# Optimization experiments

Measured on AMD Instinct MI355X. Metric: run time of the kernel, lower is better.

The kernel has to match this reference:

```python
import jax, jax.numpy as jnp
import numpy as np

B, S, E, R = 64, 2048, 256, 50


def setup_inputs() -> dict:
    key = jax.random.key(0)
    ks = jax.random.split(key, 22)
    n = lambda k, shp, s=0.05: (jax.random.normal(k, shp, jnp.float32) * s)
    d = {
        "encoder_o": jax.random.normal(ks[0], (B, S, E), jnp.float32),
        "h0": jax.random.normal(ks[1], (1, B, E), jnp.float32),
        "c0": jax.random.normal(ks[2], (1, B, E), jnp.float32),
        "r_in": jax.random.randint(ks[3], (B,), 0, R),
        "k1": jax.random.randint(ks[4], (B, 1), 0, S),
        "k2": jax.random.randint(ks[5], (B, 1), 0, S),
        "W_ih": n(ks[6], (4 * E, E)),
        "W_hh": n(ks[7], (4 * E, E)),
        "b_ih": n(ks[8], (4 * E,)),
        "b_hh": n(ks[9], (4 * E,)),
        "W_attn": n(ks[10], (E, 2 * E)),
        "b_attn": n(ks[11], (E,)),
        "W_conv": n(ks[12], (E, 2 * E, 3)),
        "b_conv": n(ks[13], (E,)),
        "sos_emb": n(ks[14], (1, E)),
        "rel_emb": n(ks[15], (R, E)),
        "W_rel": n(ks[16], (R, E)),
        "b_rel": n(ks[17], (R,)),
        "W_ent1": n(ks[18], (1, E)),
        "b_ent1": n(ks[19], (1,)),
        "W_ent2": n(ks[20], (1, E)),
        "b_ent2": n(ks[21], (1,)),
    }
    return d


def reference(encoder_o, h0, c0, r_in, k1, k2, W_ih, W_hh, b_ih, b_hh,
              W_attn, b_attn, W_conv, b_conv, sos_emb, rel_emb,
              W_rel, b_rel, W_ent1, b_ent1, W_ent2, b_ent2):
    Bx, Sx, Ex = encoder_o.shape

    def lstm_step(x, h, c):  # single decode step, x/h/c: [B,E]
        gates = x @ W_ih.T + h @ W_hh.T + (b_ih + b_hh)  # [B,4E]
        i, f, g, o = jnp.split(gates, 4, axis=-1)        # PyTorch gate order i,f,g,o
        c2 = jax.nn.sigmoid(f) * c + jax.nn.sigmoid(i) * jnp.tanh(g)
        h2 = jax.nn.sigmoid(o) * jnp.tanh(c2)
        return h2, c2

    def attend(q):  # Luong dot attention + tanh(linear(cat(mix,q))); q: [B,E]
        scores = jnp.einsum('be,bse->bs', q, encoder_o)
        attn = jax.nn.softmax(scores, axis=-1)
        mix = jnp.einsum('bs,bse->be', attn, encoder_o)
        comb = jnp.concatenate([mix, q], axis=-1)        # [B,2E]
        return jnp.tanh(comb @ W_attn.T + b_attn)

    def step(x, h, c):
        h2, c2 = lstm_step(x, h, c)
        return attend(h2), h2, c2

    kern = jnp.transpose(W_conv, (2, 1, 0))  # [3, 2E, E] for NWC/WIO

    def ent_heads(o):  # o: [B,E]
        vec = jnp.broadcast_to(o[:, None, :], (Bx, Sx, Ex))  # seq_and_vec
        feat = jnp.concatenate([encoder_o, vec], axis=-1)    # [B,S,2E]
        conv = jax.lax.conv_general_dilated(
            feat, kern, (1,), 'SAME',
            dimension_numbers=('NWC', 'WIO', 'NWC')) + b_conv
        conv = jax.nn.relu(conv)                             # [B,S,E]
        e1 = conv @ W_ent1.T + b_ent1                        # [B,S,1]
        e2 = conv @ W_ent2.T + b_ent2
        return e1, e2

    h, c = h0[0], c0[0]
    # t1: <sos> -> relation logits
    x = jnp.broadcast_to(sos_emb[0], (Bx, Ex))
    out1, h, c = step(x, h, c)
    t1_out = out1 @ W_rel.T + b_rel                          # [B,R]
    # t2: relation embedding -> entity-1 span heads
    out2, h, c = step(rel_emb[r_in], h, c)
    e1a, e2a = ent_heads(out2)
    # t3: gathered k1+k2 encoder vectors -> entity-2 span heads
    idx = jnp.arange(Bx)
    kk = encoder_o[idx, k1[:, 0]] + encoder_o[idx, k2[:, 0]]  # vectorized seq_gather
    out3, h, c = step(kk, h, c)
    e1b, e2b = ent_heads(out3)
    # pack outputs: [B, R + 4*S]
    return jnp.concatenate(
        [t1_out, e1a[..., 0], e2a[..., 0], e1b[..., 0], e2b[..., 0]], axis=1)
```

## Files before the change

kernel.cpp:

```cpp
#include <hip/hip_runtime.h>
#include <hip/hip_bf16.h>

#define EE 256
#define SS 2048
#define BB 64
#define RN 50
#define OSTR 8242

typedef __attribute__((ext_vector_type(4))) float vf4;
typedef __attribute__((ext_vector_type(8))) short s8v;
typedef __attribute__((ext_vector_type(4))) short s4v;
typedef __attribute__((ext_vector_type(4))) unsigned short u16x4;
typedef __attribute__((ext_vector_type(2))) unsigned int u32x2;

__device__ __forceinline__ unsigned short f2bf(float f){
  __hip_bfloat16 h = __float2bfloat16(f);
  return *reinterpret_cast<unsigned short*>(&h);
}
__device__ __forceinline__ unsigned int f2bf2(float a, float b){
  __hip_bfloat162 h = __float22bfloat162_rn(make_float2(a, b));
  return *reinterpret_cast<unsigned int*>(&h);
}
__device__ __forceinline__ float sigm(float x){ return 1.0f/(1.0f + __expf(-x)); }
__device__ __forceinline__ float dot4(vf4 a, vf4 b){ return a.x*b.x + a.y*b.y + a.z*b.z + a.w*b.w; }

__device__ __forceinline__ vf4 mfma16(s4v a, s4v b, vf4 c){
#if __has_builtin(__builtin_amdgcn_mfma_f32_16x16x16bf16_1k)
  return __builtin_amdgcn_mfma_f32_16x16x16bf16_1k(a, b, c, 0, 0, 0);
#else
  vf4 d;
  asm volatile("v_mfma_f32_16x16x16_bf16 %0, %1, %2, %3\n\ts_nop 7\n\ts_nop 7"
               : "=v"(d) : "v"(a), "v"(b), "v"(c));
  return d;
#endif
}

__global__ __launch_bounds__(256) void k_pre(
  const float* __restrict__ enc, const float* __restrict__ h0, const float* __restrict__ c0,
  const int* __restrict__ r_in, const int* __restrict__ k1, const int* __restrict__ k2,
  const float* __restrict__ sos, const float* __restrict__ rel,
  float* __restrict__ xT, float* __restrict__ hT0, float* __restrict__ cT)
{
  int bid = blockIdx.x, t = threadIdx.x;
  int part = bid >> 6, b = bid & 63;
  if (part == 0){
    xT[(size_t)0*EE*BB + t*BB + b] = sos[t];
  } else if (part == 1){
    xT[(size_t)1*EE*BB + t*BB + b] = rel[r_in[b]*EE + t];
  } else if (part == 2){
    int i1 = k1[b], i2 = k2[b];
    xT[(size_t)2*EE*BB + t*BB + b] =
      enc[((size_t)b*SS + i1)*EE + t] + enc[((size_t)b*SS + i2)*EE + t];
  } else {
    hT0[t*BB + b] = h0[b*EE + t];
    cT [t*BB + b] = c0[b*EE + t];
  }
}

__global__ __launch_bounds__(256) void k_step(
  const float* __restrict__ hT_cur, const float* __restrict__ xT_st,
  const float* __restrict__ W_ih, const float* __restrict__ W_hh,
  const float* __restrict__ b_ih, const float* __restrict__ b_hh,
  float* __restrict__ cT, float* __restrict__ hT_next, float* __restrict__ hs_st)
{
  int e = blockIdx.x, tid = threadIdx.x;
  int w = tid >> 6, b = tid & 63;
  int grow = w*EE + e;
  const float* wh = W_hh + (size_t)grow*EE;
  const float* wi = W_ih + (size_t)grow*EE;
  float acc = b_ih[grow] + b_hh[grow];
  #pragma unroll 4
  for (int k4 = 0; k4 < EE/4; ++k4){
    vf4 wh4 = *(const vf4*)(wh + k4*4);
    vf4 wi4 = *(const vf4*)(wi + k4*4);
    int k = k4*4;
    acc += hT_cur[(k+0)*BB+b]*wh4.x + hT_cur[(k+1)*BB+b]*wh4.y
         + hT_cur[(k+2)*BB+b]*wh4.z + hT_cur[(k+3)*BB+b]*wh4.w;
    acc += xT_st[(k+0)*BB+b]*wi4.x + xT_st[(k+1)*BB+b]*wi4.y
         + xT_st[(k+2)*BB+b]*wi4.z + xT_st[(k+3)*BB+b]*wi4.w;
  }
  __shared__ float sm[4][BB];
  sm[w][b] = acc;
  __syncthreads();
  if (tid < BB){
    float iv = sm[0][tid], fv = sm[1][tid], gv = sm[2][tid], ov = sm[3][tid];
    float cprev = cT[e*BB + tid];
    float cn = sigm(fv)*cprev + sigm(iv)*tanhf(gv);
    float hn = sigm(ov)*tanhf(cn);
    cT[e*BB + tid] = cn;
    hT_next[e*BB + tid] = hn;
    hs_st[(size_t)tid*EE + e] = hn;
  }
}

__global__ __launch_bounds__(256) void k_wprep(const float* __restrict__ W_conv,
                                               unsigned short* __restrict__ WT)
{
  int o = blockIdx.x, tid = threadIdx.x;
  for (int r = tid; r < 768; r += 256)
    WT[(size_t)r*EE + o] = f2bf(W_conv[(size_t)o*1536 + 768 + r]);
}

__global__ __launch_bounds__(256) void k_attend(
  const float* __restrict__ enc, const float* __restrict__ hs,
  float* __restrict__ mixc, float* __restrict__ stats)
{
  int bid = blockIdx.x; int b = bid >> 3, ch = bid & 7;
  int tid = threadIdx.x, lane = tid & 63, wv = tid >> 6;
  __shared__ float hsm[3][EE];
  __shared__ float wgt[3][256];
  __shared__ float red[3][4];
  __shared__ float mg[3];
  __shared__ vf4 mpart[4][3][64];
  for (int i = tid; i < 3*EE; i += 256) hsm[i>>8][i&255] = hs[((size_t)(i>>8)*BB + b)*EE + (i&255)];
  __syncthreads();
  int s = ch*256 + tid;
  const vf4* er = (const vf4*)(enc + ((size_t)b*SS + s)*EE);
  const vf4* q0 = (const vf4*)hsm[0];
  const vf4* q1 = (const vf4*)hsm[1];
  const vf4* q2 = (const vf4*)hsm[2];
  float a0=0.f, a1=0.f, a2=0.f;
  #pragma unroll 8
  for (int k = 0; k < EE/4; ++k){
    vf4 ev = er[k];
    a0 += dot4(ev, q0[k]);
    a1 += dot4(ev, q1[k]);
    a2 += dot4(ev, q2[k]);
  }
  float m0=a0, m1=a1, m2=a2;
  #pragma unroll
  for (int d=1; d<64; d<<=1){
    m0 = fmaxf(m0, __shfl_xor(m0,d));
    m1 = fmaxf(m1, __shfl_xor(m1,d));
    m2 = fmaxf(m2, __shfl_xor(m2,d));
  }
  if (lane==0){ red[0][wv]=m0; red[1][wv]=m1; red[2][wv]=m2; }
  __syncthreads();
  if (tid < 3) mg[tid] = fmaxf(fmaxf(red[tid][0],red[tid][1]), fmaxf(red[tid][2],red[tid][3]));
  __syncthreads();
  float e0 = __expf(a0-mg[0]), e1 = __expf(a1-mg[1]), e2 = __expf(a2-mg[2]);
  wgt[0][tid]=e0; wgt[1][tid]=e1; wgt[2][tid]=e2;
  #pragma unroll
  for (int d=1; d<64; d<<=1){
    e0 += __shfl_xor(e0,d); e1 += __shfl_xor(e1,d); e2 += __shfl_xor(e2,d);
  }
  if (lane==0){ red[0][wv]=e0; red[1][wv]=e1; red[2][wv]=e2; }
  __syncthreads();
  if (tid < 3){
    float l = red[tid][0]+red[tid][1]+red[tid][2]+red[tid][3];
    int o = ((tid*BB + b)*8 + ch)*2;
    stats[o] = mg[tid]; stats[o+1] = l;
  }
  __syncthreads();
  vf4 A0 = (vf4)0.0f, A1 = (vf4)0.0f, A2 = (vf4)0.0f;
  for (int i=0;i<64;++i){
    int sl = wv*64 + i;
    vf4 ev = *(const vf4*)(enc + ((size_t)b*SS + ch*256 + sl)*EE + lane*4);
    A0 += ev*wgt[0][sl]; A1 += ev*wgt[1][sl]; A2 += ev*wgt[2][sl];
  }
  mpart[wv][0][lane]=A0; mpart[wv][1][lane]=A1; mpart[wv][2][lane]=A2;
  __syncthreads();
  if (tid < 192){
    int q = tid >> 6, e4 = tid & 63;
    vf4 sum = mpart[0][q][e4] + mpart[1][q][e4] + mpart[2][q][e4] + mpart[3][q][e4];
    *(vf4*)(mixc + ((size_t)(q*BB+b)*8 + ch)*EE + e4*4) = sum;
  }
}

__global__ __launch_bounds__(256) void k_post(
  const float* __restrict__ mixc, const float* __restrict__ hs,
  const float* __restrict__ stats,
  const float* __restrict__ W_attn, const float* __restrict__ b_attn,
  const float* __restrict__ W_rel, const float* __restrict__ b_rel,
  const unsigned short* __restrict__ WT, const float* __restrict__ b_conv,
  float* __restrict__ out, float* __restrict__ vv)
{
  int b = blockIdx.x, t = threadIdx.x;
  __shared__ float comb[3][2*EE];
  __shared__ float o1[EE], o2s[EE], o3s[EE];
  #pragma unroll
  for (int q=0;q<3;q++){
    float M = -1e30f;
    #pragma unroll
    for (int c=0;c<8;c++) M = fmaxf(M, stats[((q*BB+b)*8 + c)*2]);
    float L = 0.f;
    float scl[8];
    #pragma unroll
    for (int c=0;c<8;c++){
      int o = ((q*BB+b)*8 + c)*2;
      float e = __expf(stats[o]-M);
      scl[c] = e; L += stats[o+1]*e;
    }
    float invL = 1.0f/L;
    float m = 0.f;
    #pragma unroll
    for (int c=0;c<8;c++) m += mixc[((size_t)(q*BB+b)*8 + c)*EE + t] * scl[c];
    comb[q][t] = m * invL;
    comb[q][EE+t] = hs[((size_t)q*BB + b)*EE + t];
  }
  __syncthreads();
  float a0 = b_attn[t], a1 = a0, a2 = a0;
  const vf4* wr = (const vf4*)(W_attn + (size_t)t*2*EE);
  const vf4* c0v = (const vf4*)comb[0];
  const vf4* c1v = (const vf4*)comb[1];
  const vf4* c2v = (const vf4*)comb[2];
  #pragma unroll 4
  for (int k=0;k<2*EE/4;++k){
    vf4 w = wr[k];
    a0 += dot4(w, c0v[k]); a1 += dot4(w, c1v[k]); a2 += dot4(w, c2v[k]);
  }
  o1[t]=tanhf(a0); o2s[t]=tanhf(a1); o3s[t]=tanhf(a2);
  __syncthreads();
  if (t < RN){
    float acc = b_rel[t];
    const vf4* wrel = (const vf4*)(W_rel + (size_t)t*EE);
    const vf4* ov = (const vf4*)o1;
    for (int k=0;k<EE/4;++k) acc += dot4(wrel[k], ov[k]);
    out[(size_t)b*OSTR + t] = acc;
  }
  float va0=0,va1=0,va2=0, vb0=0,vb1=0,vb2=0;
  for (int i=0;i<EE;++i){
    float x2 = o2s[i], x3 = o3s[i];
    const unsigned short* wt = WT + (size_t)i*3*EE + t;
    float w0 = __uint_as_float(((unsigned int)wt[0]) << 16);
    float w1 = __uint_as_float(((unsigned int)wt[EE]) << 16);
    float w2 = __uint_as_float(((unsigned int)wt[2*EE]) << 16);
    va0 += x2*w0; va1 += x2*w1; va2 += x2*w2;
    vb0 += x3*w0; vb1 += x3*w1; vb2 += x3*w2;
  }
  float bc = b_conv[t];
  vv[((0*3+0)*BB + b)*EE + t] = va0+va1+va2+bc;
  vv[((0*3+1)*BB + b)*EE + t] = va1+va2+bc;
  vv[((0*3+2)*BB + b)*EE + t] = va0+va1+bc;
  vv[((1*3+0)*BB + b)*EE + t] = vb0+vb1+vb2+bc;
  vv[((1*3+1)*BB + b)*EE + t] = vb1+vb2+bc;
  vv[((1*3+2)*BB + b)*EE + t] = vb0+vb1+bc;
}

__global__ __launch_bounds__(256) void k_bprep(const float* __restrict__ W_conv,
                                               unsigned short* __restrict__ Bp)
{
  int gid = blockIdx.x*256 + threadIdx.x;
  int kc  = gid >> 10;
  int rem = gid & 1023;
  int ni  = rem >> 6;
  int l   = rem & 63;
  int o   = ni*16 + (l & 15);
  int kbase = kc*32 + ((l >> 4) << 3);
  u16x4 lo4, hi4;
  #pragma unroll
  for (int j=0;j<8;++j){
    int k = kbase + j; int ktap = k >> 8; int i = k & 255;
    unsigned short v = f2bf(W_conv[((size_t)o*512 + i)*3 + ktap]);
    if (j<4){ if(j==0)lo4.x=v; else if(j==1)lo4.y=v; else if(j==2)lo4.z=v; else lo4.w=v; }
    else    { if(j==4)hi4.x=v; else if(j==5)hi4.y=v; else if(j==6)hi4.z=v; else hi4.w=v; }
  }
  u16x4* dst = (u16x4*)(Bp + (size_t)gid*8);
  dst[0] = lo4; dst[1] = hi4;
}

__global__ __launch_bounds__(256, 3) void k_conv(
  const float* __restrict__ enc, const unsigned short* __restrict__ Bp,
  const float* __restrict__ vv,
  const float* __restrict__ W_e1, const float* __restrict__ b_e1,
  const float* __restrict__ W_e2, const float* __restrict__ b_e2,
  float* __restrict__ out)
{
  int stile = blockIdx.x, b = blockIdx.y;
  int s0 = stile*64;
  int tid = threadIdx.x, lane = tid & 63, w = tid >> 6;
  int lo = lane & 15, hi = lane >> 4;
  __shared__ __align__(16) unsigned short Ab[66*256];
  __shared__ float part2[4][64][4];

  {
    const float* eb = enc + (size_t)b*SS*EE;
    for (int idx = tid; idx < 66*64; idx += 256){
      int r = idx >> 6, c4 = idx & 63;
      int s = s0 - 1 + r;
      vf4 v = (vf4)0.0f;
      if (s >= 0 && s < SS) v = *(const vf4*)(eb + (size_t)s*EE + c4*4);
      u32x2 pk; pk.x = f2bf2(v.x, v.y); pk.y = f2bf2(v.z, v.w);
      int byte = (r*512 + c4*8) ^ ((r & 7) << 4);
      *(u32x2*)((char*)Ab + byte) = pk;
    }
  }
  __syncthreads();

  vf4 acc[4][4];
  #pragma unroll
  for (int oi=0;oi<4;++oi){
    #pragma unroll
    for (int si=0;si<4;++si) acc[oi][si] = (vf4)0.0f;
  }
  const s8v* Bp8 = (const s8v*)Bp;
  s8v bf[4], bfn[4];
  #pragma unroll
  for (int oi=0;oi<4;++oi) bf[oi] = Bp8[((0*16 + (w*4+oi)) << 6) + lane];

  for (int kc=0; kc<24; ++kc){
    int ktap = kc >> 3;
    int colb = ((kc & 7) << 6) + (hi << 4);
    s8v af[4];
    #pragma unroll
    for (int si=0;si<4;++si){
      int row = si*16 + lo + ktap;
      int byte = row*512 + (colb ^ ((row & 7) << 4));
      af[si] = *(const s8v*)((const char*)Ab + byte);
    }
    if (kc < 23){
      #pragma unroll
      for (int oi=0;oi<4;++oi) bfn[oi] = Bp8[(((kc+1)*16 + (w*4+oi)) << 6) + lane];
    }
    #pragma unroll
    for (int oi=0;oi<4;++oi){
      #pragma unroll
      for (int si=0;si<4;++si)
        acc[oi][si] = __builtin_amdgcn_mfma_f32_16x16x32_bf16(bf[oi], af[si], acc[oi][si], 0, 0, 0);
    }
    #pragma unroll
    for (int oi=0;oi<4;++oi) bf[oi] = bfn[oi];
  }

  bool firstTile = (s0 == 0), lastTile = (s0 + 64 == SS);
  vf4 vaI[4], vbI[4]; s4v aw[4];
  #pragma unroll
  for (int oi=0;oi<4;++oi){
    int o4 = w*64 + oi*16 + hi*4;
    vaI[oi] = *(const vf4*)(vv + ((0*3+0)*BB + b)*EE + o4);
    vbI[oi] = *(const vf4*)(vv + ((1*3+0)*BB + b)*EE + o4);
    vf4 w1 = *(const vf4*)(W_e1 + o4);
    vf4 w2 = *(const vf4*)(W_e2 + o4);
    float e0 = (lo==0) ? w1.x : ((lo==1) ? w2.x : 0.0f);
    float e1 = (lo==0) ? w1.y : ((lo==1) ? w2.y : 0.0f);
    float e2 = (lo==0) ? w1.z : ((lo==1) ? w2.z : 0.0f);
    float e3 = (lo==0) ? w1.w : ((lo==1) ? w2.w : 0.0f);
    u32x2 t; t.x = f2bf2(e0, e1); t.y = f2bf2(e2, e3);
    aw[oi] = __builtin_bit_cast(s4v, t);
  }
  #pragma unroll
  for (int si=0; si<4; ++si){
    vf4 Da = (vf4)0.0f, Db = (vf4)0.0f;
    #pragma unroll
    for (int oi=0; oi<4; ++oi){
      int o4 = w*64 + oi*16 + hi*4;
      vf4 c = acc[oi][si];
      vf4 va = vaI[oi], vb = vbI[oi];
      if (firstTile && si==0 && lo==0){
        va = *(const vf4*)(vv + ((0*3+1)*BB + b)*EE + o4);
        vb = *(const vf4*)(vv + ((1*3+1)*BB + b)*EE + o4);
      }
      if (lastTile && si==3 && lo==15){
        va = *(const vf4*)(vv + ((0*3+2)*BB + b)*EE + o4);
        vb = *(const vf4*)(vv + ((1*3+2)*BB + b)*EE + o4);
      }
      float a0 = fmaxf(c.x+va.x,0.f), a1 = fmaxf(c.y+va.y,0.f);
      float a2 = fmaxf(c.z+va.z,0.f), a3 = fmaxf(c.w+va.w,0.f);
      float b0 = fmaxf(c.x+vb.x,0.f), b1 = fmaxf(c.y+vb.y,0.f);
      float b2 = fmaxf(c.z+vb.z,0.f), b3 = fmaxf(c.w+vb.w,0.f);
      u32x2 ta; ta.x = f2bf2(a0,a1); ta.y = f2bf2(a2,a3);
      u32x2 tb; tb.x = f2bf2(b0,b1); tb.y = f2bf2(b2,b3);
      Da = mfma16(aw[oi], __builtin_bit_cast(s4v, ta), Da);
      Db = mfma16(aw[oi], __builtin_bit_cast(s4v, tb), Db);
    }
    if (hi == 0){
      vf4 pk; pk.x = Da.x; pk.y = Da.y; pk.z = Db.x; pk.w = Db.y;
      *(vf4*)&part2[w][si*16+lo][0] = pk;
    }
  }
  __syncthreads();
  {
    int s = tid >> 2, c = tid & 3;
    float r = part2[0][s][c] + part2[1][s][c] + part2[2][s][c] + part2[3][s][c];
    r += (c & 1) ? b_e2[0] : b_e1[0];
    out[(size_t)b*OSTR + RN + c*SS + (s0 + s)] = r;
  }
}

extern "C" void kernel_launch(void* const* d_in, const int* in_sizes, int n_in,
                              void* d_out, int out_size, void* d_ws, size_t ws_size,
                              hipStream_t stream)
{
  const float* enc   = (const float*)d_in[0];
  const float* h0    = (const float*)d_in[1];
  const float* c0    = (const float*)d_in[2];
  const int*   r_in  = (const int*)d_in[3];
  const int*   k1    = (const int*)d_in[4];
  const int*   k2    = (const int*)d_in[5];
  const float* W_ih  = (const float*)d_in[6];
  const float* W_hh  = (const float*)d_in[7];
  const float* b_ih  = (const float*)d_in[8];
  const float* b_hh  = (const float*)d_in[9];
  const float* W_attn= (const float*)d_in[10];
  const float* b_attn= (const float*)d_in[11];
  const float* W_conv= (const float*)d_in[12];
  const float* b_conv= (const float*)d_in[13];
  const float* sos   = (const float*)d_in[14];
  const float* rel   = (const float*)d_in[15];
  const float* W_rel = (const float*)d_in[16];
  const float* b_rel = (const float*)d_in[17];
  const float* W_e1  = (const float*)d_in[18];
  const float* b_e1  = (const float*)d_in[19];
  const float* W_e2  = (const float*)d_in[20];
  const float* b_e2  = (const float*)d_in[21];
  float* out = (float*)d_out;
  char* ws = (char*)d_ws;

  float* hs    = (float*)(ws);
  float* vv    = (float*)(ws + 196608);
  float* stats = (float*)(ws + 589824);
  float* mixc  = (float*)(ws + 602112);
  unsigned short* Bp = (unsigned short*)(ws + 2174976);
  float* xT    = (float*)(ws + 2568192);
  float* hTa   = (float*)(ws + 2764800);
  float* hTb   = (float*)(ws + 2830336);
  float* cT    = (float*)(ws + 2895872);
  unsigned short* WT = (unsigned short*)(ws + 2568192);

  hipLaunchKernelGGL(k_pre,   dim3(256), dim3(256), 0, stream,
                     enc,h0,c0,r_in,k1,k2,sos,rel, xT,hTa,cT);
  hipLaunchKernelGGL(k_step,  dim3(256), dim3(256), 0, stream,
                     hTa, xT + 0*EE*BB, W_ih,W_hh,b_ih,b_hh, cT, hTb, hs + 0*BB*EE);
  hipLaunchKernelGGL(k_step,  dim3(256), dim3(256), 0, stream,
                     hTb, xT + 1*EE*BB, W_ih,W_hh,b_ih,b_hh, cT, hTa, hs + 1*BB*EE);
  hipLaunchKernelGGL(k_step,  dim3(256), dim3(256), 0, stream,
                     hTa, xT + 2*EE*BB, W_ih,W_hh,b_ih,b_hh, cT, hTb, hs + 2*BB*EE);
  hipLaunchKernelGGL(k_wprep, dim3(256), dim3(256), 0, stream, W_conv, WT);
  hipLaunchKernelGGL(k_attend,dim3(512), dim3(256), 0, stream, enc, hs, mixc, stats);
  hipLaunchKernelGGL(k_post,  dim3(64),  dim3(256), 0, stream,
                     mixc, hs, stats, W_attn,b_attn, W_rel,b_rel, WT, b_conv, out, vv);
  hipLaunchKernelGGL(k_bprep, dim3(96),  dim3(256), 0, stream, W_conv, Bp);
  hipLaunchKernelGGL(k_conv,  dim3(32,64), dim3(256), 0, stream,
                     enc, Bp, vv, W_e1,b_e1, W_e2,b_e2, out);
}
```

Before: 220.1 us.

## Emit bf16 swizzled encoder copy in attend and async-load it in conv

The attend kernel already streams the fp32 encoder, so it now also writes a pre-swizzled bf16 copy into workspace. The conv kernel then fills its LDS tile from that half-size copy with direct global-to-LDS loads instead of re-reading fp32 and converting. The two weight-prep kernels are also merged into the input-prep kernel to cut launches. The trade is an extra 64 MB bf16 write during attend. The new path only runs when the workspace is large enough and otherwise falls back to the old fp32 path.

```diff
diff --git a/kernel.cpp b/kernel.cpp
--- a/kernel.cpp
+++ b/kernel.cpp
@@ -35,25 +35,57 @@
 #endif
 }
 
-__global__ __launch_bounds__(256) void k_pre(
+__device__ __forceinline__ void gload_lds16(const void* g, void* l){
+  __builtin_amdgcn_global_load_lds(
+      (const __attribute__((address_space(1))) unsigned int*)g,
+      (__attribute__((address_space(3))) unsigned int*)l, 16, 0, 0);
+}
+
+__global__ __launch_bounds__(256) void k_prep(
   const float* __restrict__ enc, const float* __restrict__ h0, const float* __restrict__ c0,
   const int* __restrict__ r_in, const int* __restrict__ k1, const int* __restrict__ k2,
   const float* __restrict__ sos, const float* __restrict__ rel,
-  float* __restrict__ xT, float* __restrict__ hT0, float* __restrict__ cT)
+  const float* __restrict__ W_conv,
+  float* __restrict__ xT, float* __restrict__ hT0, float* __restrict__ cT,
+  unsigned short* __restrict__ WT, unsigned short* __restrict__ Bp)
 {
   int bid = blockIdx.x, t = threadIdx.x;
-  int part = bid >> 6, b = bid & 63;
-  if (part == 0){
-    xT[(size_t)0*EE*BB + t*BB + b] = sos[t];
-  } else if (part == 1){
-    xT[(size_t)1*EE*BB + t*BB + b] = rel[r_in[b]*EE + t];
-  } else if (part == 2){
-    int i1 = k1[b], i2 = k2[b];
-    xT[(size_t)2*EE*BB + t*BB + b] =
-      enc[((size_t)b*SS + i1)*EE + t] + enc[((size_t)b*SS + i2)*EE + t];
+  if (bid < 256){
+    int part = bid >> 6, b = bid & 63;
+    if (part == 0){
+      xT[(size_t)0*EE*BB + t*BB + b] = sos[t];
+    } else if (part == 1){
+      xT[(size_t)1*EE*BB + t*BB + b] = rel[r_in[b]*EE + t];
+    } else if (part == 2){
+      int i1 = k1[b], i2 = k2[b];
+      xT[(size_t)2*EE*BB + t*BB + b] =
+        enc[((size_t)b*SS + i1)*EE + t] + enc[((size_t)b*SS + i2)*EE + t];
+    } else {
+      hT0[t*BB + b] = h0[b*EE + t];
+      cT [t*BB + b] = c0[b*EE + t];
+    }
+  } else if (bid < 512){
+    int o = bid - 256;
+    for (int r = t; r < 768; r += 256)
+      WT[(size_t)r*EE + o] = f2bf(W_conv[(size_t)o*1536 + 768 + r]);
   } else {
-    hT0[t*BB + b] = h0[b*EE + t];
-    cT [t*BB + b] = c0[b*EE + t];
+    int gid = (bid - 512)*256 + t;
+    int kc  = gid >> 10;
+    int rem = gid & 1023;
+    int ni  = rem >> 6;
+    int l   = rem & 63;
+    int o   = ni*16 + (l & 15);
+    int kbase = kc*32 + ((l >> 4) << 3);
+    u16x4 lo4, hi4;
+    #pragma unroll
+    for (int j=0;j<8;++j){
+      int k = kbase + j; int ktap = k >> 8; int i = k & 255;
+      unsigned short v = f2bf(W_conv[((size_t)o*512 + i)*3 + ktap]);
+      if (j<4){ if(j==0)lo4.x=v; else if(j==1)lo4.y=v; else if(j==2)lo4.z=v; else lo4.w=v; }
+      else    { if(j==4)hi4.x=v; else if(j==5)hi4.y=v; else if(j==6)hi4.z=v; else hi4.w=v; }
+    }
+    u16x4* dst = (u16x4*)(Bp + (size_t)gid*8);
+    dst[0] = lo4; dst[1] = hi4;
   }
 }
 
@@ -93,17 +125,10 @@
   }
 }
 
-__global__ __launch_bounds__(256) void k_wprep(const float* __restrict__ W_conv,
-                                               unsigned short* __restrict__ WT)
-{
-  int o = blockIdx.x, tid = threadIdx.x;
-  for (int r = tid; r < 768; r += 256)
-    WT[(size_t)r*EE + o] = f2bf(W_conv[(size_t)o*1536 + 768 + r]);
-}
-
 __global__ __launch_bounds__(256) void k_attend(
   const float* __restrict__ enc, const float* __restrict__ hs,
-  float* __restrict__ mixc, float* __restrict__ stats)
+  float* __restrict__ mixc, float* __restrict__ stats,
+  unsigned short* __restrict__ encb)
 {
   int bid = blockIdx.x; int b = bid >> 3, ch = bid & 7;
   int tid = threadIdx.x, lane = tid & 63, wv = tid >> 6;
@@ -155,7 +180,13 @@
   vf4 A0 = (vf4)0.0f, A1 = (vf4)0.0f, A2 = (vf4)0.0f;
   for (int i=0;i<64;++i){
     int sl = wv*64 + i;
-    vf4 ev = *(const vf4*)(enc + ((size_t)b*SS + ch*256 + sl)*EE + lane*4);
+    int gs = ch*256 + sl;
+    vf4 ev = *(const vf4*)(enc + ((size_t)b*SS + gs)*EE + lane*4);
+    if (encb){
+      u32x2 pk; pk.x = f2bf2(ev.x, ev.y); pk.y = f2bf2(ev.z, ev.w);
+      int off = (lane*8) ^ (((gs + 1) & 7) << 4);
+      *(u32x2*)((char*)encb + ((size_t)b*SS + gs)*512 + off) = pk;
+    }
     A0 += ev*wgt[0][sl]; A1 += ev*wgt[1][sl]; A2 += ev*wgt[2][sl];
   }
   mpart[wv][0][lane]=A0; mpart[wv][1][lane]=A1; mpart[wv][2][lane]=A2;
@@ -237,30 +268,9 @@
   vv[((1*3+2)*BB + b)*EE + t] = vb0+vb1+bc;
 }
 
-__global__ __launch_bounds__(256) void k_bprep(const float* __restrict__ W_conv,
-                                               unsigned short* __restrict__ Bp)
-{
-  int gid = blockIdx.x*256 + threadIdx.x;
-  int kc  = gid >> 10;
-  int rem = gid & 1023;
-  int ni  = rem >> 6;
-  int l   = rem & 63;
-  int o   = ni*16 + (l & 15);
-  int kbase = kc*32 + ((l >> 4) << 3);
-  u16x4 lo4, hi4;
-  #pragma unroll
-  for (int j=0;j<8;++j){
-    int k = kbase + j; int ktap = k >> 8; int i = k & 255;
-    unsigned short v = f2bf(W_conv[((size_t)o*512 + i)*3 + ktap]);
-    if (j<4){ if(j==0)lo4.x=v; else if(j==1)lo4.y=v; else if(j==2)lo4.z=v; else lo4.w=v; }
-    else    { if(j==4)hi4.x=v; else if(j==5)hi4.y=v; else if(j==6)hi4.z=v; else hi4.w=v; }
-  }
-  u16x4* dst = (u16x4*)(Bp + (size_t)gid*8);
-  dst[0] = lo4; dst[1] = hi4;
-}
-
 __global__ __launch_bounds__(256, 3) void k_conv(
-  const float* __restrict__ enc, const unsigned short* __restrict__ Bp,
+  const float* __restrict__ enc, const unsigned short* __restrict__ encb,
+  const unsigned short* __restrict__ Bp,
   const float* __restrict__ vv,
   const float* __restrict__ W_e1, const float* __restrict__ b_e1,
   const float* __restrict__ W_e2, const float* __restrict__ b_e2,
@@ -273,7 +283,24 @@
   __shared__ __align__(16) unsigned short Ab[66*256];
   __shared__ float part2[4][64][4];
 
-  {
+  if (encb){
+    const char* ebase = (const char*)encb + (size_t)b*SS*512;
+    for (int base = 0; base < 66*32; base += 256){
+      int idx = base + tid;
+      if (idx < 66*32){
+        int r = idx >> 5, c = idx & 31;
+        int srow = s0 - 1 + r;
+        srow = srow < 0 ? 0 : (srow > SS-1 ? SS-1 : srow);
+        gload_lds16(ebase + (size_t)srow*512 + c*16, (char*)Ab + idx*16);
+      }
+    }
+    __syncthreads();
+    if (stile == 0 || stile == 31){
+      if (stile == 0  && tid < 32) *(vf4*)((char*)Ab + tid*16) = (vf4)0.0f;
+      if (stile == 31 && tid < 32) *(vf4*)((char*)Ab + 65*512 + tid*16) = (vf4)0.0f;
+      __syncthreads();
+    }
+  } else {
     const float* eb = enc + (size_t)b*SS*EE;
     for (int idx = tid; idx < 66*64; idx += 256){
       int r = idx >> 6, c4 = idx & 63;
@@ -284,8 +311,8 @@
       int byte = (r*512 + c4*8) ^ ((r & 7) << 4);
       *(u32x2*)((char*)Ab + byte) = pk;
     }
-  }
-  __syncthreads();
+    __syncthreads();
+  }
 
   vf4 acc[4][4];
   #pragma unroll
@@ -415,21 +442,22 @@
   float* hTa   = (float*)(ws + 2764800);
   float* hTb   = (float*)(ws + 2830336);
   float* cT    = (float*)(ws + 2895872);
-  unsigned short* WT = (unsigned short*)(ws + 2568192);
-
-  hipLaunchKernelGGL(k_pre,   dim3(256), dim3(256), 0, stream,
-                     enc,h0,c0,r_in,k1,k2,sos,rel, xT,hTa,cT);
+  unsigned short* WT = (unsigned short*)(ws + 2961408);
+  size_t encb_off = 3354624;
+  size_t need = encb_off + (size_t)BB*SS*EE*2;
+  unsigned short* encb = (ws_size >= need) ? (unsigned short*)(ws + encb_off) : nullptr;
+
+  hipLaunchKernelGGL(k_prep,  dim3(608), dim3(256), 0, stream,
+                     enc,h0,c0,r_in,k1,k2,sos,rel,W_conv, xT,hTa,cT, WT,Bp);
   hipLaunchKernelGGL(k_step,  dim3(256), dim3(256), 0, stream,
                      hTa, xT + 0*EE*BB, W_ih,W_hh,b_ih,b_hh, cT, hTb, hs + 0*BB*EE);
   hipLaunchKernelGGL(k_step,  dim3(256), dim3(256), 0, stream,
                      hTb, xT + 1*EE*BB, W_ih,W_hh,b_ih,b_hh, cT, hTa, hs + 1*BB*EE);
   hipLaunchKernelGGL(k_step,  dim3(256), dim3(256), 0, stream,
                      hTa, xT + 2*EE*BB, W_ih,W_hh,b_ih,b_hh, cT, hTb, hs + 2*BB*EE);
-  hipLaunchKernelGGL(k_wprep, dim3(256), dim3(256), 0, stream, W_conv, WT);
-  hipLaunchKernelGGL(k_attend,dim3(512), dim3(256), 0, stream, enc, hs, mixc, stats);
+  hipLaunchKernelGGL(k_attend,dim3(512), dim3(256), 0, stream, enc, hs, mixc, stats, encb);
   hipLaunchKernelGGL(k_post,  dim3(64),  dim3(256), 0, stream,
                      mixc, hs, stats, W_attn,b_attn, W_rel,b_rel, WT, b_conv, out, vv);
-  hipLaunchKernelGGL(k_bprep, dim3(96),  dim3(256), 0, stream, W_conv, Bp);
   hipLaunchKernelGGL(k_conv,  dim3(32,64), dim3(256), 0, stream,
-                     enc, Bp, vv, W_e1,b_e1, W_e2,b_e2, out);
-}
+                     enc, encb, Bp, vv, W_e1,b_e1, W_e2,b_e2, out);
+}
```

Result: no change. 217.5 us (-1.2%).
